# Kernel tuning notes

Hardware: AMD Instinct MI355X
Metric: run time of the kernel (lower is better)

Reference implementation:

```python
import jax, jax.numpy as jnp
import numpy as np

B, N, D, H = 8, 512, 1024, 16
HD = D // H
NI = 4          # num_instances == num_instances_per_batch
MAXI = 16       # max_instances
SCALE = HD ** -0.5


def _rms(t, w, eps=1e-6):
    return t * jax.lax.rsqrt(jnp.mean(t * t, axis=-1, keepdims=True) + eps) * w


def _lin(t, W, b):
    return t @ W + b


def _heads(t):
    b, n = t.shape[0], t.shape[1]
    return t.reshape(b, n, H, HD).transpose(0, 2, 1, 3)  # [b, H, n, hd]


def setup_inputs() -> dict:
    key = jax.random.key(0)
    ks = iter(jax.random.split(key, 16))

    def w(shape):
        return jax.random.normal(next(ks), shape, dtype=jnp.float32) * 0.02

    return {
        "x": jax.random.normal(next(ks), (B, N, D), dtype=jnp.float32),
        "instance_mask": jax.random.uniform(next(ks), (B, N, NI), dtype=jnp.float32),
        "Wq": w((D, D)), "bq": jnp.zeros((D,), jnp.float32),
        "Wk": w((D, D)), "bk": jnp.zeros((D,), jnp.float32),
        "Wv": w((D, D)), "bv": jnp.zeros((D,), jnp.float32),
        "Wo": w((D, D)), "bo": jnp.zeros((D,), jnp.float32),
        "Wiq": w((D, D)), "biq": jnp.zeros((D,), jnp.float32),
        "Wik": w((D, D)), "bik": jnp.zeros((D,), jnp.float32),
        "instance_embed": w((1, MAXI, D)),
        "qnorm_w": jnp.ones((HD,), jnp.float32),
        "knorm_w": jnp.ones((HD,), jnp.float32),
        "num_instances": NI,
        "num_instances_per_batch": NI,
    }


def reference(x, instance_mask, Wq, bq, Wk, bk, Wv, bv, Wo, bo,
              Wiq, biq, Wik, bik, instance_embed, qnorm_w, knorm_w,
              num_instances, num_instances_per_batch):
    # QKV projections + per-head QK-RMSNorm
    q = _rms(_heads(_lin(x, Wq, bq)), qnorm_w)   # [B,H,N,hd]
    k = _rms(_heads(_lin(x, Wk, bk)), knorm_w)
    v = _heads(_lin(x, Wv, bv))
    ni = num_instances                           # == num_instances_per_batch here,
    G = B // num_instances_per_batch             # so no leftover self-attn sub-branch;
    # (the module's initial global attention output is overwritten by this branch)
    qg = q.reshape(G, ni, H, N, HD)
    kg = k.reshape(G, ni, H, N, HD).transpose(0, 2, 1, 3, 4).reshape(G, H, ni * N, HD)
    vg = v.reshape(G, ni, H, N, HD).transpose(0, 2, 1, 3, 4).reshape(G, H, ni * N, HD)
    scores = jnp.einsum('gihnd,ghmd->gihnm', qg, kg) * SCALE  # [G,ni,H,N,ni*N]
    p = jax.nn.softmax(scores, axis=-1)
    og = jnp.einsum('gihnm,ghmd->gihnd', p, vg)
    out = og.reshape(B, H, N, HD).transpose(0, 2, 1, 3).reshape(B, N, D)
    # instance-embedding gate
    inst_feat = jnp.einsum('bnk,kd->bnd', instance_mask, instance_embed[0, :ni])
    iq = _heads(_lin(out, Wiq, biq))
    ik = _heads(_lin(inst_feat, Wik, bik))
    # mean over heads folded into the einsum (same math as mean of per-head scores)
    inst_attn = jax.nn.sigmoid(jnp.einsum('bhnd,bhmd->bnm', iq, ik) * (SCALE / H))
    gate = 1.0 + jnp.mean(inst_attn, axis=-1, keepdims=True)  # [B,N,1]
    return _lin(out * gate, Wo, bo)
```

## Files before the change

### kernel.cpp

```cpp
#include <hip/hip_runtime.h>
#include <cmath>

#define B_   8
#define N_   512
#define D_   1024
#define H_   16
#define HD_  64
#define NI_  4
#define BN_  (B_*N_)
#define KVLEN (NI_*N_)

typedef __attribute__((ext_vector_type(8)))  short  bf16x8;
typedef __attribute__((ext_vector_type(8)))  __bf16 bf16x8_t;
typedef __attribute__((ext_vector_type(16))) float  f32x16;
typedef __attribute__((ext_vector_type(4)))  short  s16x4;
typedef __attribute__((ext_vector_type(2)))  unsigned u32x2;

__device__ __forceinline__ short bf16_rn(float x) {
  unsigned u = __float_as_uint(x);
  unsigned r = (u + 0x7FFFu + ((u >> 16) & 1u)) >> 16;
  return (short)r;
}

__device__ __forceinline__ f32x16 mfma_bf16(bf16x8 a, bf16x8 b, f32x16 c) {
  return __builtin_amdgcn_mfma_f32_32x32x16_bf16(
      __builtin_bit_cast(bf16x8_t, a), __builtin_bit_cast(bf16x8_t, b), c, 0, 0, 0);
}

#define GLOAD16(gp, lp) __builtin_amdgcn_global_load_lds( \
  (const __attribute__((address_space(1))) unsigned*)(gp), \
  (__attribute__((address_space(3))) unsigned*)(lp), 16, 0, 0)

__device__ __forceinline__ long tiled_off(int row, int k) {
  return ((((long)(row >> 7) * 128 + (k >> 3)) * 128 + (row & 127)) * 8 + (k & 7));
}

__device__ __forceinline__ void xcd_swizzle(int& bx, int& by, int& bz) {
  const int gx = gridDim.x, gy = gridDim.y;
  const int nwg = gx * gy * gridDim.z;
  const int lin = blockIdx.x + gx * (blockIdx.y + gy * blockIdx.z);
  const int swz = (lin & 7) * (nwg >> 3) + (lin >> 3);
  bx = swz % gx;
  const int rest = swz / gx;
  by = rest % gy;
  bz = rest / gy;
}

__global__ __launch_bounds__(256) void wsplitAll(
    const float* __restrict__ Wq, const float* __restrict__ Wk,
    const float* __restrict__ Wv, const float* __restrict__ Wo,
    const float* __restrict__ x,
    short* __restrict__ QKVh, short* __restrict__ WoH,
    short* __restrict__ Xh)
{
  const int z = blockIdx.z;
  const int t  = threadIdx.x;
  if (z >= 4) {
    const int rowB = (z - 4) * 1024 + blockIdx.y * 64;
    const int colB = blockIdx.x * 64;
    const int r0 = t >> 4;
    const int c4 = t & 15;
    #pragma unroll
    for (int i = 0; i < 4; i++) {
      const int row = rowB + r0 + i * 16;
      float4 v = *(const float4*)&x[(long)row * D_ + colB + c4 * 4];
      short h[4];
      h[0] = bf16_rn(v.x);  h[1] = bf16_rn(v.y);
      h[2] = bf16_rn(v.z);  h[3] = bf16_rn(v.w);
      *(s16x4*)&Xh[tiled_off(row, colB + c4 * 4)] = *(s16x4*)h;
    }
    return;
  }
  __shared__ float tile[64][65];
  const float* W = (z == 0) ? Wq : (z == 1) ? Wk : (z == 2) ? Wv : Wo;
  const int kb = blockIdx.y * 64;
  const int cb = blockIdx.x * 64;
  const int r0 = t >> 4;
  const int c4 = t & 15;
  #pragma unroll
  for (int i = 0; i < 4; i++) {
    const int r = r0 + i * 16;
    *(float4*)&tile[r][c4 * 4] = *(const float4*)&W[(long)(kb + r) * D_ + cb + c4 * 4];
  }
  __syncthreads();
  #pragma unroll
  for (int i = 0; i < 4; i++) {
    const int c = r0 + i * 16;
    short hi[4];
    #pragma unroll
    for (int e = 0; e < 4; e++)
      hi[e] = bf16_rn(tile[c4 * 4 + e][c]);
    if (z < 3)
      *(s16x4*)&QKVh[tiled_off(z * D_ + cb + c, kb + c4 * 4)] = *(s16x4*)hi;
    else
      *(s16x4*)&WoH[tiled_off(cb + c, kb + c4 * 4)] = *(s16x4*)hi;
  }
}

__global__ __launch_bounds__(256) void fprep_p(
    const float* __restrict__ Wik, const float* __restrict__ emb,
    float* __restrict__ F4p)
{
  const int d  = blockIdx.x * 256 + threadIdx.x;
  const int eb = blockIdx.y;
  float s0 = 0, s1 = 0, s2 = 0, s3 = 0;
  for (int e = eb * 16; e < eb * 16 + 16; e++) {
    const float w = Wik[(long)e * D_ + d];
    s0 = fmaf(emb[e], w, s0);
    s1 = fmaf(emb[D_ + e], w, s1);
    s2 = fmaf(emb[2 * D_ + e], w, s2);
    s3 = fmaf(emb[3 * D_ + e], w, s3);
  }
  float* p = F4p + (long)eb * 4 * D_;
  p[d] = s0;  p[D_ + d] = s1;  p[2 * D_ + d] = s2;  p[3 * D_ + d] = s3;
}

__global__ __launch_bounds__(256) void freduce(
    const float* __restrict__ F4p, float* __restrict__ F4)
{
  const int i = blockIdx.x * 256 + threadIdx.x;
  float s = 0.f;
  #pragma unroll
  for (int eb = 0; eb < 64; eb++) s += F4p[(long)eb * 4096 + i];
  F4[i] = s;
}

__global__ __launch_bounds__(256) void hprep2(
    const float* __restrict__ Wiq, const float* __restrict__ F4,
    const float* __restrict__ bik, const float* __restrict__ biq,
    float* __restrict__ H5)
{
  __shared__ float red[4][5];
  const int t = threadIdx.x;
  const int blk = blockIdx.x;
  float s[5] = {0.f, 0.f, 0.f, 0.f, 0.f};
  const float* vr = (blk < 1024) ? Wiq + (long)blk * D_ : biq;
  for (int e = t; e < D_; e += 256) {
    const float w = vr[e];
    s[0] = fmaf(w, F4[e], s[0]);
    s[1] = fmaf(w, F4[D_ + e], s[1]);
    s[2] = fmaf(w, F4[2 * D_ + e], s[2]);
    s[3] = fmaf(w, F4[3 * D_ + e], s[3]);
    s[4] = fmaf(w, bik[e], s[4]);
  }
  #pragma unroll
  for (int j = 0; j < 5; j++)
    #pragma unroll
    for (int m = 1; m < 64; m <<= 1) s[j] += __shfl_xor(s[j], m);
  const int w64 = t >> 6, lane = t & 63;
  if (lane == 0)
    #pragma unroll
    for (int j = 0; j < 5; j++) red[w64][j] = s[j];
  __syncthreads();
  if (t < 5)
    H5[(long)blk * 5 + t] = red[0][t] + red[1][t] + red[2][t] + red[3][t];
}

template<int MODE, int SPLIT>
__global__ __launch_bounds__(256) void mfgemm2(
    const short* __restrict__ Ahi, const short* __restrict__ Alo,
    const short* __restrict__ Bhi,
    const float* __restrict__ b0, const float* __restrict__ b1,
    const float* __restrict__ b2,
    float* __restrict__ C, short* __restrict__ Vout,
    int bBlk, long sC, const float* __restrict__ gate_in)
{
  constexpr int NOPS = 2;
  __shared__ short lds[2][NOPS][4096];
  const int t = threadIdx.x, w = t >> 6, lane = t & 63;
  int bx, by, bz;
  xcd_swizzle(bx, by, bz);
  const int rowBase = by * 128;
  const int colBase = bx * 128;
  const long aoff = (long)by * 131072;
  const long boff = (long)(bz * bBlk + bx) * 131072;

  const int op = w >> 1, half = w & 1;
  const short* mySrc = op ? Bhi + boff : Ahi + aoff;

  auto stage = [&](int buf, int tt) {
    const short* g = mySrc + ((long)tt * 512 + half * 256 + lane) * 8;
    #pragma unroll
    for (int i = 0; i < 4; i++)
      GLOAD16(g + i * 512, &lds[buf][op][(half * 256 + i * 64) * 8]);
  };

  const int wr = w >> 1, wc = w & 1;
  const int lrow = lane & 31, lk = lane >> 5;

  f32x16 acc[2][2] = {};

  auto compute = [&](int buf) {
    #pragma unroll
    for (int kh = 0; kh < 2; kh++) {
      const int kq = 2 * kh + lk;
      bf16x8 ah[2], bh[2];
      #pragma unroll
      for (int m = 0; m < 2; m++)
        ah[m] = *(const bf16x8*)&lds[buf][0][(kq * 128 + wr * 64 + m * 32 + lrow) * 8];
      #pragma unroll
      for (int n = 0; n < 2; n++)
        bh[n] = *(const bf16x8*)&lds[buf][1][(kq * 128 + wc * 64 + n * 32 + lrow) * 8];
      #pragma unroll
      for (int m = 0; m < 2; m++)
        #pragma unroll
        for (int n = 0; n < 2; n++)
          acc[m][n] = mfma_bf16(ah[m], bh[n], acc[m][n]);
    }
  };

  const int NT = 32;
  stage(0, 0);
  for (int tt = 0; tt < NT - 1; ++tt) {
    stage((tt + 1) & 1, tt + 1);
    asm volatile("s_waitcnt vmcnt(4)" ::: "memory");
    __builtin_amdgcn_s_barrier();
    __builtin_amdgcn_sched_barrier(0);
    compute(tt & 1);
    __builtin_amdgcn_s_barrier();
  }
  asm volatile("s_waitcnt vmcnt(0)" ::: "memory");
  __builtin_amdgcn_s_barrier();
  __builtin_amdgcn_sched_barrier(0);
  compute((NT - 1) & 1);

  const float* bias = (bz == 1) ? b1 : (bz == 2) ? b2 : b0;
  float bcol[2];
  #pragma unroll
  for (int n = 0; n < 2; n++)
    bcol[n] = bias[colBase + wc * 64 + n * 32 + lrow];

  if (MODE == 6 && bz == 2) {
    #pragma unroll
    for (int m = 0; m < 2; m++)
      #pragma unroll
      for (int r = 0; r < 16; r++) {
        const int row = rowBase + wr * 64 + m * 32 + (r & 3) + 8 * (r >> 2) + 4 * lk;
        const int bb = row >> 9, g = bb >> 2;
        const int kv = (bb & 3) * 512 + (row & 511);
        const int tile = kv >> 5, vkv = kv & 31;
        #pragma unroll
        for (int n = 0; n < 2; n++) {
          const int col = colBase + wc * 64 + n * 32 + lrow;
          const int h = col >> 6, dl = col & 63;
          const long idx = ((long)(g * H_ + h) * 64 + tile) * 2048
                         + dl * 32 + (((vkv >> 3) ^ ((dl >> 1) & 3)) * 8) + (vkv & 7);
          Vout[idx] = bf16_rn(acc[m][n][r] + bcol[n]);
        }
      }
    return;
  }

  float* Cb = C + (long)bz * sC;
  #pragma unroll
  for (int m = 0; m < 2; m++) {
    #pragma unroll
    for (int r = 0; r < 16; r++) {
      const int row = rowBase + wr * 64 + m * 32 + (r & 3) + 8 * (r >> 2) + 4 * lk;
      float g = 1.f;
      if (MODE == 2) g = gate_in[row];
      #pragma unroll
      for (int n = 0; n < 2; n++) {
        const int col = colBase + wc * 64 + n * 32 + lrow;
        Cb[(long)row * D_ + col] = acc[m][n][r] * g + bcol[n];
      }
    }
  }
}

__global__ __launch_bounds__(256) void kvprepK(
    const float* __restrict__ kf, const float* __restrict__ knw,
    short* __restrict__ Knb)
{
  const int tile = blockIdx.x, h = blockIdx.y, g = blockIdx.z;
  const int t = threadIdx.x;
  const int skv = t >> 3, sg = t & 7;
  const int m  = tile * 32 + skv;
  const int bb = g * NI_ + (m >> 9), nn = m & (N_ - 1);
  const float* kp = kf + ((long)(bb * N_ + nn)) * D_ + h * HD_ + sg * 8;
  float k8[8];
  *(float4*)&k8[0] = *(const float4*)&kp[0];
  *(float4*)&k8[4] = *(const float4*)&kp[4];
  float ks2 = 0.f;
  #pragma unroll
  for (int j = 0; j < 8; j++) ks2 += k8[j] * k8[j];
  ks2 += __shfl_xor(ks2, 1);
  ks2 += __shfl_xor(ks2, 2);
  ks2 += __shfl_xor(ks2, 4);
  const float kr = rsqrtf(ks2 * (1.f / 64.f) + 1e-6f);
  bf16x8 kb;
  #pragma unroll
  for (int j = 0; j < 8; j++) kb[j] = bf16_rn(k8[j] * kr * knw[sg * 8 + j]);
  *(bf16x8*)&Knb[((long)(g * H_ + h) * KVLEN + m) * 64 + ((sg ^ (m & 7)) * 8)] = kb;
}

__global__ __launch_bounds__(256) void attn3(
    const float* __restrict__ q, const short* __restrict__ Knb,
    const short* __restrict__ Vtb, const float* __restrict__ qnw,
    float* __restrict__ opart, float* __restrict__ lpart)
{
  int qb, h, bz;
  xcd_swizzle(qb, h, bz);
  const int b  = bz / 3, s = bz - 3 * b;
  const int g  = b >> 2;
  const int t  = threadIdx.x;
  const int w  = t >> 6;
  const int lane = t & 63;
  const int l31 = lane & 31, hi = lane >> 5;

  __shared__ short Kt[2][2048];
  __shared__ short Vt[2][2048];

  const int qrow = qb * 128 + w * 32 + l31;
  const float* qp = q + ((long)b * N_ + qrow) * D_ + h * HD_ + hi * 8;
  float qv[4][8];
  float ss = 0.f;
  #pragma unroll
  for (int c = 0; c < 4; c++) {
    *(float4*)&qv[c][0] = *(const float4*)&qp[c * 16];
    *(float4*)&qv[c][4] = *(const float4*)&qp[c * 16 + 4];
    #pragma unroll
    for (int j = 0; j < 8; j++) ss += qv[c][j] * qv[c][j];
  }
  ss += __shfl_xor(ss, 32);
  const float qr = rsqrtf(ss * (1.f / 64.f) + 1e-6f) * 0.1803368801111244f;
  bf16x8 qf[4];
  #pragma unroll
  for (int c = 0; c < 4; c++)
    #pragma unroll
    for (int j = 0; j < 8; j++)
      qf[c][j] = bf16_rn(qv[c][j] * qr * qnw[c * 16 + hi * 8 + j]);

  const short* Kg = Knb + (long)(g * H_ + h) * KVLEN * 64;
  const short* Vg = Vtb + (long)(g * H_ + h) * 64 * 2048;

  auto stage = [&](int buf, int i) {
    GLOAD16(Kg + (long)i * 2048 + t * 8, &Kt[buf][w * 512]);
    GLOAD16(Vg + (long)i * 2048 + t * 8, &Vt[buf][w * 512]);
  };

  const int it0 = (s * 64) / 3;
  const int it1 = ((s + 1) * 64) / 3;

  f32x16 oacc[2] = {};
  float l = 0.f;

  stage(0, it0);
  for (int i = it0; i < it1; ++i) {
    const int buf = (i - it0) & 1;
    if (i + 1 < it1) {
      stage(buf ^ 1, i + 1);
      asm volatile("s_waitcnt vmcnt(2)" ::: "memory");
    } else {
      asm volatile("s_waitcnt vmcnt(0)" ::: "memory");
    }
    __builtin_amdgcn_s_barrier();
    __builtin_amdgcn_sched_barrier(0);

    f32x16 sc = {};
    #pragma unroll
    for (int c = 0; c < 4; c++) {
      bf16x8 kfr = *(const bf16x8*)&Kt[buf][l31 * 64 + (((2 * c + hi) * 8) ^ ((l31 & 7) << 3))];
      sc = mfma_bf16(kfr, qf[c], sc);
    }
    float p[16];
    #pragma unroll
    for (int r = 0; r < 16; r++) {
      p[r] = exp2f(sc[r]);
      l += p[r];
    }
    unsigned wd[8];
    #pragma unroll
    for (int i2 = 0; i2 < 8; i2++)
      asm("v_cvt_pk_bf16_f32 %0, %1, %2" : "=v"(wd[i2]) : "v"(p[2 * i2]), "v"(p[2 * i2 + 1]));
    u32x2 r0 = __builtin_amdgcn_permlane32_swap(wd[0], wd[2], false, false);
    u32x2 r1 = __builtin_amdgcn_permlane32_swap(wd[1], wd[3], false, false);
    u32x2 r2 = __builtin_amdgcn_permlane32_swap(wd[4], wd[6], false, false);
    u32x2 r3 = __builtin_amdgcn_permlane32_swap(wd[5], wd[7], false, false);
    int4 f0 = { (int)r0.x, (int)r1.x, (int)r0.y, (int)r1.y };
    int4 f1 = { (int)r2.x, (int)r3.x, (int)r2.y, (int)r3.y };
    #pragma unroll
    for (int n = 0; n < 2; n++) {
      const int d = n * 32 + l31;
      const int fd = (d >> 1) & 3;
      bf16x8 v0 = *(const bf16x8*)&Vt[buf][d * 32 + ((hi ^ fd) * 8)];
      bf16x8 v1 = *(const bf16x8*)&Vt[buf][d * 32 + (((2 | hi) ^ fd) * 8)];
      oacc[n] = mfma_bf16(__builtin_bit_cast(bf16x8, f0), v0, oacc[n]);
      oacc[n] = mfma_bf16(__builtin_bit_cast(bf16x8, f1), v1, oacc[n]);
    }
    __builtin_amdgcn_s_barrier();
  }

  l += __shfl_xor(l, 32);
  #pragma unroll
  for (int r = 0; r < 16; r++) {
    const int qg = qb * 128 + w * 32 + (r & 3) + 8 * (r >> 2) + 4 * hi;
    float* op = opart + ((long)s * BN_ + b * N_ + qg) * D_ + h * HD_ + l31;
    op[0]  = oacc[0][r];
    op[32] = oacc[1][r];
  }
  if (hi == 0)
    lpart[((long)s * BN_ + b * N_ + qb * 128 + w * 32 + l31) * H_ + h] = l;
}

__global__ __launch_bounds__(256) void attn_reduce2(
    const float* __restrict__ opart, const float* __restrict__ lpart,
    const float* __restrict__ H5, const float* __restrict__ mask,
    short* __restrict__ ohi, float* __restrict__ gate)
{
  __shared__ float red[4][5];
  __shared__ float Gs[5];
  __shared__ float sred[4];
  const int t = threadIdx.x;
  const int row = blockIdx.x;
  const int bb = row >> 9;
  const int col = t * 4;
  const int h   = col >> 6;
  const float l = lpart[(long)row * H_ + h]
                + lpart[((long)BN_ + row) * H_ + h]
                + lpart[((long)2 * BN_ + row) * H_ + h];
  const float inv = 1.f / l;
  float4 a = *(const float4*)&opart[(long)row * D_ + col];
  float4 b = *(const float4*)&opart[((long)BN_ + row) * D_ + col];
  float4 c = *(const float4*)&opart[((long)2 * BN_ + row) * D_ + col];
  float o4[4] = { (a.x + b.x + c.x) * inv, (a.y + b.y + c.y) * inv,
                  (a.z + b.z + c.z) * inv, (a.w + b.w + c.w) * inv };
  short hh[4];
  hh[0] = bf16_rn(o4[0]);  hh[1] = bf16_rn(o4[1]);
  hh[2] = bf16_rn(o4[2]);  hh[3] = bf16_rn(o4[3]);
  *(s16x4*)&ohi[tiled_off(row, col)] = *(s16x4*)hh;
  float s[5] = {0.f, 0.f, 0.f, 0.f, 0.f};
  #pragma unroll
  for (int cc = 0; cc < 4; cc++) {
    const float* hp = &H5[(long)(col + cc) * 5];
    #pragma unroll
    for (int j = 0; j < 5; j++) s[j] = fmaf(o4[cc], hp[j], s[j]);
  }
  #pragma unroll
  for (int j = 0; j < 5; j++)
    #pragma unroll
    for (int m = 1; m < 64; m <<= 1) s[j] += __shfl_xor(s[j], m);
  const int w64 = t >> 6, lane = t & 63;
  if (lane == 0)
    #pragma unroll
    for (int j = 0; j < 5; j++) red[w64][j] = s[j];
  __syncthreads();
  if (t < 5) Gs[t] = red[0][t] + red[1][t] + red[2][t] + red[3][t] + H5[5120 + t];
  __syncthreads();
  const float g0 = Gs[0], g1 = Gs[1], g2 = Gs[2], g3 = Gs[3], g4 = Gs[4];
  const float sc = 0.125f / 16.f;
  const float* mrow = mask + (long)bb * N_ * NI_;
  float sg = 0.f;
  #pragma unroll
  for (int q = 0; q < 2; q++) {
    const float4 mk = *(const float4*)&mrow[(t * 2 + q) * 4];
    const float z = fmaf(g0, mk.x, fmaf(g1, mk.y, fmaf(g2, mk.z, fmaf(g3, mk.w, g4))));
    sg += 1.f / (1.f + __expf(-z * sc));
  }
  #pragma unroll
  for (int m = 1; m < 64; m <<= 1) sg += __shfl_xor(sg, m);
  if (lane == 0) sred[w64] = sg;
  __syncthreads();
  if (t == 0)
    gate[row] = 1.f + (sred[0] + sred[1] + sred[2] + sred[3]) * (1.f / 512.f);
}

extern "C" void kernel_launch(void* const* d_in, const int* in_sizes, int n_in,
                              void* d_out, int out_size, void* d_ws, size_t ws_size,
                              hipStream_t stream)
{
  const float* x    = (const float*)d_in[0];
  const float* mask = (const float*)d_in[1];
  const float* Wq   = (const float*)d_in[2];
  const float* bq   = (const float*)d_in[3];
  const float* Wk   = (const float*)d_in[4];
  const float* bk   = (const float*)d_in[5];
  const float* Wv   = (const float*)d_in[6];
  const float* bv   = (const float*)d_in[7];
  const float* Wo   = (const float*)d_in[8];
  const float* bo   = (const float*)d_in[9];
  const float* Wiq  = (const float*)d_in[10];
  const float* biq  = (const float*)d_in[11];
  const float* Wik  = (const float*)d_in[12];
  const float* bik  = (const float*)d_in[13];
  const float* emb  = (const float*)d_in[14];
  const float* qnw  = (const float*)d_in[15];
  const float* knw  = (const float*)d_in[16];
  float* out = (float*)d_out;

  float* ws = (float*)d_ws;
  const size_t SZ = (size_t)BN_ * D_;
  float* qbuf = ws;
  float* kbuf = qbuf + SZ;
  float* opart = kbuf;
  short* ohi  = (short*)qbuf;
  short* xhi  = (short*)(ws + 4 * SZ);
  short* xlo  = xhi + SZ;
  short* Knb  = xhi;
  short* Vtb  = xlo;
  short* Wbig_hi = (short*)(ws + 5 * SZ);
  short* Wbig_lo = Wbig_hi + (size_t)3 * D_ * D_;
  float* gate  = (float*)Wbig_hi;
  float* lpart = gate + BN_;
  short* WoH = Wbig_lo;
  float* F4  = (float*)(Wbig_lo + (size_t)D_ * D_);
  float* H5  = F4 + 4 * D_;
  float* F4p = H5 + 1025 * 5;

  const dim3 blk(256);

  fprep_p<<<dim3(4, 64), blk, 0, stream>>>(Wik, emb, F4p);
  freduce<<<dim3(16), blk, 0, stream>>>(F4p, F4);
  hprep2<<<dim3(1025), blk, 0, stream>>>(Wiq, F4, bik, biq, H5);

  wsplitAll<<<dim3(16, 16, 8), blk, 0, stream>>>(
      Wq, Wk, Wv, Wo, x, Wbig_hi, WoH, xhi);

  mfgemm2<6, 0><<<dim3(8, 32, 3), blk, 0, stream>>>(
      xhi, nullptr, Wbig_hi, bq, bk, bv,
      qbuf, Vtb, 8, (long)SZ, nullptr);

  kvprepK<<<dim3(KVLEN / 32, H_, 2), blk, 0, stream>>>(kbuf, knw, Knb);

  attn3<<<dim3(N_ / 128, H_, B_ * 3), blk, 0, stream>>>(
      qbuf, Knb, Vtb, qnw, opart, lpart);

  attn_reduce2<<<BN_, blk, 0, stream>>>(opart, lpart, H5, mask, ohi, gate);

  mfgemm2<2, 0><<<dim3(8, 32, 1), blk, 0, stream>>>(
      ohi, nullptr, WoH, bo, nullptr, nullptr,
      out, nullptr, 0, 0, gate);
}
```

Before: 188.7 us.

## Fuse K RMSNorm into QKV GEMM epilogue and split attention KV in halves

The QKV GEMM epilogue for the K slice now computes the per-head RMS norm with cross-lane shuffles and writes swizzled bf16 K straight into the attention layout. This removes the separate kvprepK kernel and the fp32 K round trip through memory. Attention also changes its KV split from three uneven parts to two equal halves of 32 tiles, and the reduce kernel now sums two partials. The trade is fewer attention blocks (less parallelism) and scattered 2-byte stores in the GEMM epilogue.

```diff
diff --git a/kernel.cpp b/kernel.cpp
--- a/kernel.cpp
+++ b/kernel.cpp
@@ -156,17 +156,16 @@
     H5[(long)blk * 5 + t] = red[0][t] + red[1][t] + red[2][t] + red[3][t];
 }
 
-template<int MODE, int SPLIT>
+template<int MODE>
 __global__ __launch_bounds__(256) void mfgemm2(
-    const short* __restrict__ Ahi, const short* __restrict__ Alo,
-    const short* __restrict__ Bhi,
+    const short* __restrict__ Ahi, const short* __restrict__ Bhi,
     const float* __restrict__ b0, const float* __restrict__ b1,
     const float* __restrict__ b2,
     float* __restrict__ C, short* __restrict__ Vout,
+    short* __restrict__ Kout, const float* __restrict__ knw,
     int bBlk, long sC, const float* __restrict__ gate_in)
 {
-  constexpr int NOPS = 2;
-  __shared__ short lds[2][NOPS][4096];
+  __shared__ short lds[2][2][4096];
   const int t = threadIdx.x, w = t >> 6, lane = t & 63;
   int bx, by, bz;
   xcd_swizzle(bx, by, bz);
@@ -251,6 +250,34 @@
     return;
   }
 
+  if (MODE == 6 && bz == 1) {
+    const float kw0 = knw[lrow];
+    const float kw1 = knw[32 + lrow];
+    const int h = (colBase + wc * 64) >> 6;
+    #pragma unroll
+    for (int m = 0; m < 2; m++)
+      #pragma unroll
+      for (int r = 0; r < 16; r++) {
+        const int row = rowBase + wr * 64 + m * 32 + (r & 3) + 8 * (r >> 2) + 4 * lk;
+        const int bb = row >> 9, g = bb >> 2;
+        const int mkv = (bb & 3) * 512 + (row & 511);
+        const float v0 = acc[m][0][r] + bcol[0];
+        const float v1 = acc[m][1][r] + bcol[1];
+        float ks2 = v0 * v0 + v1 * v1;
+        ks2 += __shfl_xor(ks2, 1);
+        ks2 += __shfl_xor(ks2, 2);
+        ks2 += __shfl_xor(ks2, 4);
+        ks2 += __shfl_xor(ks2, 8);
+        ks2 += __shfl_xor(ks2, 16);
+        const float kr = rsqrtf(ks2 * (1.f / 64.f) + 1e-6f);
+        const long base = ((long)(g * H_ + h) * KVLEN + mkv) * 64;
+        const int d0 = lrow, d1 = 32 + lrow;
+        Kout[base + (((d0 >> 3) ^ (mkv & 7)) << 3) + (d0 & 7)] = bf16_rn(v0 * kr * kw0);
+        Kout[base + (((d1 >> 3) ^ (mkv & 7)) << 3) + (d1 & 7)] = bf16_rn(v1 * kr * kw1);
+      }
+    return;
+  }
+
   float* Cb = C + (long)bz * sC;
   #pragma unroll
   for (int m = 0; m < 2; m++) {
@@ -268,32 +295,6 @@
   }
 }
 
-__global__ __launch_bounds__(256) void kvprepK(
-    const float* __restrict__ kf, const float* __restrict__ knw,
-    short* __restrict__ Knb)
-{
-  const int tile = blockIdx.x, h = blockIdx.y, g = blockIdx.z;
-  const int t = threadIdx.x;
-  const int skv = t >> 3, sg = t & 7;
-  const int m  = tile * 32 + skv;
-  const int bb = g * NI_ + (m >> 9), nn = m & (N_ - 1);
-  const float* kp = kf + ((long)(bb * N_ + nn)) * D_ + h * HD_ + sg * 8;
-  float k8[8];
-  *(float4*)&k8[0] = *(const float4*)&kp[0];
-  *(float4*)&k8[4] = *(const float4*)&kp[4];
-  float ks2 = 0.f;
-  #pragma unroll
-  for (int j = 0; j < 8; j++) ks2 += k8[j] * k8[j];
-  ks2 += __shfl_xor(ks2, 1);
-  ks2 += __shfl_xor(ks2, 2);
-  ks2 += __shfl_xor(ks2, 4);
-  const float kr = rsqrtf(ks2 * (1.f / 64.f) + 1e-6f);
-  bf16x8 kb;
-  #pragma unroll
-  for (int j = 0; j < 8; j++) kb[j] = bf16_rn(k8[j] * kr * knw[sg * 8 + j]);
-  *(bf16x8*)&Knb[((long)(g * H_ + h) * KVLEN + m) * 64 + ((sg ^ (m & 7)) * 8)] = kb;
-}
-
 __global__ __launch_bounds__(256) void attn3(
     const float* __restrict__ q, const short* __restrict__ Knb,
     const short* __restrict__ Vtb, const float* __restrict__ qnw,
@@ -301,7 +302,7 @@
 {
   int qb, h, bz;
   xcd_swizzle(qb, h, bz);
-  const int b  = bz / 3, s = bz - 3 * b;
+  const int b  = bz >> 1, s = bz & 1;
   const int g  = b >> 2;
   const int t  = threadIdx.x;
   const int w  = t >> 6;
@@ -331,24 +332,21 @@
     for (int j = 0; j < 8; j++)
       qf[c][j] = bf16_rn(qv[c][j] * qr * qnw[c * 16 + hi * 8 + j]);
 
-  const short* Kg = Knb + (long)(g * H_ + h) * KVLEN * 64;
-  const short* Vg = Vtb + (long)(g * H_ + h) * 64 * 2048;
+  const short* Kg = Knb + (long)(g * H_ + h) * KVLEN * 64 + (long)s * 32 * 2048;
+  const short* Vg = Vtb + (long)(g * H_ + h) * 64 * 2048 + (long)s * 32 * 2048;
 
   auto stage = [&](int buf, int i) {
     GLOAD16(Kg + (long)i * 2048 + t * 8, &Kt[buf][w * 512]);
     GLOAD16(Vg + (long)i * 2048 + t * 8, &Vt[buf][w * 512]);
   };
 
-  const int it0 = (s * 64) / 3;
-  const int it1 = ((s + 1) * 64) / 3;
-
   f32x16 oacc[2] = {};
   float l = 0.f;
 
-  stage(0, it0);
-  for (int i = it0; i < it1; ++i) {
-    const int buf = (i - it0) & 1;
-    if (i + 1 < it1) {
+  stage(0, 0);
+  for (int i = 0; i < 32; ++i) {
+    const int buf = i & 1;
+    if (i + 1 < 32) {
       stage(buf ^ 1, i + 1);
       asm volatile("s_waitcnt vmcnt(2)" ::: "memory");
     } else {
@@ -416,15 +414,12 @@
   const int bb = row >> 9;
   const int col = t * 4;
   const int h   = col >> 6;
-  const float l = lpart[(long)row * H_ + h]
-                + lpart[((long)BN_ + row) * H_ + h]
-                + lpart[((long)2 * BN_ + row) * H_ + h];
+  const float l = lpart[(long)row * H_ + h] + lpart[((long)BN_ + row) * H_ + h];
   const float inv = 1.f / l;
   float4 a = *(const float4*)&opart[(long)row * D_ + col];
   float4 b = *(const float4*)&opart[((long)BN_ + row) * D_ + col];
-  float4 c = *(const float4*)&opart[((long)2 * BN_ + row) * D_ + col];
-  float o4[4] = { (a.x + b.x + c.x) * inv, (a.y + b.y + c.y) * inv,
-                  (a.z + b.z + c.z) * inv, (a.w + b.w + c.w) * inv };
+  float o4[4] = { (a.x + b.x) * inv, (a.y + b.y) * inv,
+                  (a.z + b.z) * inv, (a.w + b.w) * inv };
   short hh[4];
   hh[0] = bf16_rn(o4[0]);  hh[1] = bf16_rn(o4[1]);
   hh[2] = bf16_rn(o4[2]);  hh[3] = bf16_rn(o4[3]);
@@ -491,13 +486,11 @@
   float* ws = (float*)d_ws;
   const size_t SZ = (size_t)BN_ * D_;
   float* qbuf = ws;
-  float* kbuf = qbuf + SZ;
-  float* opart = kbuf;
+  float* opart = ws + SZ;
   short* ohi  = (short*)qbuf;
+  short* Knb  = (short*)(ws + 3 * SZ);
   short* xhi  = (short*)(ws + 4 * SZ);
-  short* xlo  = xhi + SZ;
-  short* Knb  = xhi;
-  short* Vtb  = xlo;
+  short* Vtb  = xhi + SZ;
   short* Wbig_hi = (short*)(ws + 5 * SZ);
   short* Wbig_lo = Wbig_hi + (size_t)3 * D_ * D_;
   float* gate  = (float*)Wbig_hi;
@@ -516,18 +509,16 @@
   wsplitAll<<<dim3(16, 16, 8), blk, 0, stream>>>(
       Wq, Wk, Wv, Wo, x, Wbig_hi, WoH, xhi);
 
-  mfgemm2<6, 0><<<dim3(8, 32, 3), blk, 0, stream>>>(
-      xhi, nullptr, Wbig_hi, bq, bk, bv,
-      qbuf, Vtb, 8, (long)SZ, nullptr);
-
-  kvprepK<<<dim3(KVLEN / 32, H_, 2), blk, 0, stream>>>(kbuf, knw, Knb);
-
-  attn3<<<dim3(N_ / 128, H_, B_ * 3), blk, 0, stream>>>(
+  mfgemm2<6><<<dim3(8, 32, 3), blk, 0, stream>>>(
+      xhi, Wbig_hi, bq, bk, bv,
+      qbuf, Vtb, Knb, knw, 8, (long)SZ, nullptr);
+
+  attn3<<<dim3(N_ / 128, H_, B_ * 2), blk, 0, stream>>>(
       qbuf, Knb, Vtb, qnw, opart, lpart);
 
   attn_reduce2<<<BN_, blk, 0, stream>>>(opart, lpart, H5, mask, ohi, gate);
 
-  mfgemm2<2, 0><<<dim3(8, 32, 1), blk, 0, stream>>>(
-      ohi, nullptr, WoH, bo, nullptr, nullptr,
-      out, nullptr, 0, 0, gate);
-}
+  mfgemm2<2><<<dim3(8, 32, 1), blk, 0, stream>>>(
+      ohi, WoH, bo, nullptr, nullptr,
+      out, nullptr, nullptr, nullptr, 0, 0, gate);
+}
```

Result: faster. 182.8 us (-3.1%).
